# Performance work log

Measured on AMD Instinct MI355X. Metric: run time of the kernel, lower is better.

Reference implementation:

```python
import jax, jax.numpy as jnp
import numpy as np

SCALE = 64.0
DROP_P = 0.1


def setup_inputs() -> dict:
    key = jax.random.key(0)
    kq, kk, kv = jax.random.split(key, 3)
    B, Lq, Lk, D = 16, 2048, 2048, 64
    q_mat = jax.random.normal(kq, (B, Lq, D), dtype=jnp.float32)
    k_mat = jax.random.normal(kk, (B, Lk, D), dtype=jnp.float32)
    v_mat = jax.random.normal(kv, (B, Lk, D), dtype=jnp.float32)
    return {"q_mat": q_mat, "k_mat": k_mat, "v_mat": v_mat}


def reference(q_mat, k_mat, v_mat):
    # scores: [B, Lq, Lk]; note scale is a MULTIPLIER, as in the torch module
    scores = jnp.einsum('bqd,bkd->bqk', q_mat, k_mat) * SCALE
    # softmax over dim=-2, i.e. over the QUERY axis (non-standard)
    weights = jax.nn.softmax(scores, axis=-2)
    # dropout with p=0.1, training=True (fixed key for reproducibility)
    keep = jax.random.bernoulli(jax.random.key(42), 1.0 - DROP_P, weights.shape)
    weights = jnp.where(keep, weights / (1.0 - DROP_P), 0.0)
    # output: [B, Lq, D]
    return jnp.einsum('bqk,bkd->bqd', weights, v_mat)
```

## Files before the change

kernel.cpp:

```cpp
#include <hip/hip_runtime.h>
#include <stdint.h>


#define LQ 2048
#define DD 64

typedef short bf16x8 __attribute__((ext_vector_type(8)));
typedef float f32x4 __attribute__((ext_vector_type(4)));
typedef unsigned short ushort_t;

#define MFMA16(a, b, c) __builtin_amdgcn_mfma_f32_16x16x32_bf16(a, b, c, 0, 0, 0)

__device__ __forceinline__ ushort_t f2bf(float x) {
  uint32_t u = __float_as_uint(x);
  return (ushort_t)((u + 0x7FFFu + ((u >> 16) & 1u)) >> 16);
}
__device__ __forceinline__ float bf2f(ushort_t h) {
  return __uint_as_float(((uint32_t)h) << 16);
}

__device__ __forceinline__ void split8v(float4 a, float4 b, bf16x8* H, bf16x8* L) {
  float xs[8] = {a.x, a.y, a.z, a.w, b.x, b.y, b.z, b.w};
  bf16x8 h, l;
#pragma unroll
  for (int e = 0; e < 8; ++e) {
    ushort_t hh = f2bf(xs[e]);
    h[e] = (short)hh;
    l[e] = (short)f2bf(xs[e] - bf2f(hh));
  }
  *H = h; *L = l;
}

__device__ __forceinline__ f32x4 score6(bf16x8 Ah0, bf16x8 Ah1, bf16x8 Al0, bf16x8 Al1,
                                        bf16x8 Bh0, bf16x8 Bh1, bf16x8 Bl0, bf16x8 Bl1) {
  f32x4 acc = {0.f, 0.f, 0.f, 0.f};
  acc = MFMA16(Ah0, Bh0, acc);
  acc = MFMA16(Ah1, Bh1, acc);
  acc = MFMA16(Al0, Bh0, acc);
  acc = MFMA16(Al1, Bh1, acc);
  acc = MFMA16(Ah0, Bl0, acc);
  acc = MFMA16(Ah1, Bl1, acc);
  return acc;
}

__device__ __forceinline__ void stage_q(const float* __restrict__ gsrc,
                                        short (*Qh)[72], short (*Ql)[72], int tid) {
  const float4* src = (const float4*)gsrc;
#pragma unroll
  for (int i = 0; i < 4; ++i) {
    int idx = tid + (i << 8);
    int r = idx >> 4, c4 = idx & 15;
    float4 v = src[idx];
    short4 h, l;
    ushort_t t;
    t = f2bf(v.x); h.x = (short)t; l.x = (short)f2bf(v.x - bf2f(t));
    t = f2bf(v.y); h.y = (short)t; l.y = (short)f2bf(v.y - bf2f(t));
    t = f2bf(v.z); h.z = (short)t; l.z = (short)f2bf(v.z - bf2f(t));
    t = f2bf(v.w); h.w = (short)t; l.w = (short)f2bf(v.w - bf2f(t));
    *(short4*)&Qh[r][c4 * 4] = h;
    *(short4*)&Ql[r][c4 * 4] = l;
  }
}

__device__ __forceinline__ void tf_round(uint32_t& x0, uint32_t& x1, const int r) {
  x0 += x1;
  x1 = (x1 << r) | (x1 >> (32 - r));
  x1 ^= x0;
}

__device__ __forceinline__ bool keep_bit(uint32_t j) {
  const uint32_t ks1 = 42u, ks2 = 0x1BD11BDAu ^ 42u;
  uint32_t x0 = 0u;
  uint32_t x1 = j + ks1;
  tf_round(x0,x1,13); tf_round(x0,x1,15); tf_round(x0,x1,26); tf_round(x0,x1,6);
  x0 += ks1; x1 += ks2 + 1u;
  tf_round(x0,x1,17); tf_round(x0,x1,29); tf_round(x0,x1,16); tf_round(x0,x1,24);
  x0 += ks2; x1 += 0u + 2u;
  tf_round(x0,x1,13); tf_round(x0,x1,15); tf_round(x0,x1,26); tf_round(x0,x1,6);
  x0 += 0u; x1 += ks1 + 3u;
  tf_round(x0,x1,17); tf_round(x0,x1,29); tf_round(x0,x1,16); tf_round(x0,x1,24);
  x0 += ks1; x1 += ks2 + 4u;
  tf_round(x0,x1,13); tf_round(x0,x1,15); tf_round(x0,x1,26); tf_round(x0,x1,6);
  x0 += ks2; x1 += 0u + 5u;
  uint32_t bits = x0 ^ x1;
  float u = __uint_as_float((bits >> 9) | 0x3F800000u) - 1.0f;
  return u < 0.9f;
}

__global__ __launch_bounds__(256) void dotatt_colstats(
    const float* __restrict__ Q, const float* __restrict__ K,
    float* __restrict__ Mcol, float* __restrict__ Rcol) {
  __shared__ short Qh[64][72];
  __shared__ short Ql[64][72];
  const int bid = blockIdx.x;
  const int b = bid >> 5;
  const int kbase = (bid & 31) << 6;
  const int tid = threadIdx.x;
  const int lane = tid & 63;
  const int g = tid >> 6;
  const int kr = lane & 15;
  const int d0 = (lane >> 4) << 3;

  bf16x8 Bh0, Bl0, Bh1, Bl1;
  {
    const float* kp = K + ((size_t)b * LQ + kbase + (g << 4) + kr) * DD + d0;
    float4 a0 = *(const float4*)kp;
    float4 a1 = *(const float4*)(kp + 4);
    float4 a2 = *(const float4*)(kp + 32);
    float4 a3 = *(const float4*)(kp + 36);
    split8v(a0, a1, &Bh0, &Bl0);
    split8v(a2, a3, &Bh1, &Bl1);
  }

  const float* Qb = Q + (size_t)b * LQ * DD;
  float m = -1e30f, z = 0.f;

#pragma unroll 1
  for (int qt = 0; qt < 32; ++qt) {
    stage_q(Qb + (size_t)qt * 64 * DD, Qh, Ql, tid);
    __syncthreads();
    float s16[16];
#pragma unroll
    for (int qtile = 0; qtile < 4; ++qtile) {
      const int row = (qtile << 4) + kr;
      bf16x8 Ah0 = *(const bf16x8*)&Qh[row][d0];
      bf16x8 Ah1 = *(const bf16x8*)&Qh[row][d0 + 32];
      bf16x8 Al0 = *(const bf16x8*)&Ql[row][d0];
      bf16x8 Al1 = *(const bf16x8*)&Ql[row][d0 + 32];
      f32x4 s = score6(Ah0, Ah1, Al0, Al1, Bh0, Bh1, Bl0, Bl1);
#pragma unroll
      for (int r = 0; r < 4; ++r) s16[(qtile << 2) + r] = s[r] * 64.f;
    }
    __syncthreads();
    float mx = s16[0];
#pragma unroll
    for (int i = 1; i < 16; ++i) mx = fmaxf(mx, s16[i]);
    if (!__all(mx < m - 20.f)) {
      float mn = fmaxf(m, mx);
      float zz = 0.f;
#pragma unroll
      for (int i = 0; i < 16; ++i) zz += __expf(s16[i] - mn);
      z = z * __expf(m - mn) + zz;
      m = mn;
    }
  }
#pragma unroll
  for (int off = 16; off < 64; off <<= 1) {
    float om = __shfl_xor(m, off);
    float oz = __shfl_xor(z, off);
    float mn = fmaxf(m, om);
    z = z * __expf(m - mn) + oz * __expf(om - mn);
    m = mn;
  }
  if (lane < 16) {
    size_t o = (size_t)b * LQ + kbase + (g << 4) + lane;
    Mcol[o] = m;
    Rcol[o] = 1.0f / (0.9f * z);
  }
}

__global__ __launch_bounds__(256) void dotatt_out(
    const float* __restrict__ Q, const float* __restrict__ K,
    const float* __restrict__ V,
    const float* __restrict__ Mcol, const float* __restrict__ Rcol,
    float* __restrict__ Out) {
  __shared__ short Qh[64][72];
  __shared__ short Ql[64][72];
  __shared__ float Slds[4][64][17];

  const int bid = blockIdx.x;
  const int b = bid >> 5;
  const int qbase = (bid & 31) << 6;
  const int tid = threadIdx.x;
  const int lane = tid & 63;
  const int g = tid >> 6;
  const int kr = lane & 15;
  const int d0 = (lane >> 4) << 3;

  stage_q(Q + ((size_t)b * LQ + qbase) * DD, Qh, Ql, tid);
  __syncthreads();

  float acc[64];
#pragma unroll
  for (int d = 0; d < 64; ++d) acc[d] = 0.f;

  const float* Kb = K + (size_t)b * LQ * DD;
  const float* Vb = V + (size_t)b * LQ * DD;
  const float* Mb = Mcol + (size_t)b * LQ;
  const float* Rb = Rcol + (size_t)b * LQ;
  const uint32_t jrow = ((uint32_t)b * LQ + (uint32_t)(qbase + lane)) * (uint32_t)LQ;

#pragma unroll 1
  for (int t = 0; t < 32; ++t) {
    const int k0 = (g << 9) + (t << 4);
    bf16x8 Bh0, Bl0, Bh1, Bl1;
    {
      const float* kp = Kb + (size_t)(k0 + kr) * DD + d0;
      float4 a0 = *(const float4*)kp;
      float4 a1 = *(const float4*)(kp + 4);
      float4 a2 = *(const float4*)(kp + 32);
      float4 a3 = *(const float4*)(kp + 36);
      split8v(a0, a1, &Bh0, &Bl0);
      split8v(a2, a3, &Bh1, &Bl1);
    }
    const float Mw = Mb[k0 + kr];
    const float rr = Rb[k0 + kr];

    float sm[16];
#pragma unroll
    for (int qtile = 0; qtile < 4; ++qtile) {
      const int row = (qtile << 4) + kr;
      bf16x8 Ah0 = *(const bf16x8*)&Qh[row][d0];
      bf16x8 Ah1 = *(const bf16x8*)&Qh[row][d0 + 32];
      bf16x8 Al0 = *(const bf16x8*)&Ql[row][d0];
      bf16x8 Al1 = *(const bf16x8*)&Ql[row][d0 + 32];
      f32x4 s = score6(Ah0, Ah1, Al0, Al1, Bh0, Bh1, Bl0, Bl1);
#pragma unroll
      for (int r = 0; r < 4; ++r) sm[(qtile << 2) + r] = s[r] * 64.f - Mw;
    }
    float mx = sm[0];
#pragma unroll
    for (int i = 1; i < 16; ++i) mx = fmaxf(mx, sm[i]);
    if (__all(mx < -25.f)) continue;

#pragma unroll
    for (int qtile = 0; qtile < 4; ++qtile)
#pragma unroll
      for (int r = 0; r < 4; ++r)
        Slds[g][(qtile << 4) + ((lane >> 4) << 2) + r][kr] = sm[(qtile << 2) + r];

#pragma unroll 1
    for (int kk = 0; kk < 16; ++kk) {
      float smv = Slds[g][lane][kk];
      if (__all(smv < -25.f)) continue;
      float Rk = __shfl(rr, kk);
      float w = __expf(smv) * Rk;
      if (!keep_bit(jrow + (uint32_t)(k0 + kk))) w = 0.f;
      const float4* vrow = (const float4*)(Vb + (size_t)(k0 + kk) * DD);
#pragma unroll
      for (int c4 = 0; c4 < 16; ++c4) {
        float4 vv = vrow[c4];
        acc[4 * c4 + 0] += w * vv.x;
        acc[4 * c4 + 1] += w * vv.y;
        acc[4 * c4 + 2] += w * vv.z;
        acc[4 * c4 + 3] += w * vv.w;
      }
    }
  }

  __syncthreads();
  float (*qs)[68] = (float(*)[68])&Slds[0][0][0];
  for (int gg = 0; gg < 4; ++gg) {
    if (g == gg) {
      if (gg == 0) {
#pragma unroll
        for (int d = 0; d < 64; ++d) qs[lane][d] = acc[d];
      } else {
#pragma unroll
        for (int d = 0; d < 64; ++d) qs[lane][d] += acc[d];
      }
    }
    __syncthreads();
  }

  float* Ob = Out + ((size_t)b * LQ + qbase) * DD;
#pragma unroll
  for (int i = 0; i < 4; ++i) {
    int idx = tid + (i << 8);
    int r = idx >> 4, c4 = idx & 15;
    ((float4*)Ob)[idx] = *(const float4*)&qs[r][c4 * 4];
  }
}

extern "C" void kernel_launch(void* const* d_in, const int* in_sizes, int n_in,
                              void* d_out, int out_size, void* d_ws, size_t ws_size,
                              hipStream_t stream) {
  const float* Q = (const float*)d_in[0];
  const float* K = (const float*)d_in[1];
  const float* V = (const float*)d_in[2];
  float* Out  = (float*)d_out;
  float* Mcol = (float*)d_ws;
  float* Rcol = Mcol + (size_t)16 * LQ;

  hipLaunchKernelGGL(dotatt_colstats, dim3(16 * 32), dim3(256), 0, stream,
                     Q, K, Mcol, Rcol);
  hipLaunchKernelGGL(dotatt_out, dim3(16 * 32), dim3(256), 0, stream,
                     Q, K, V, Mcol, Rcol, Out);
}
```

Measured before the change: 206.0 us.

## Pre-split Q/K into bf16 hi/lo once and widen attention kernels to 512 threads

Adds a pre-pass kernel that converts Q and K into bf16 high/low halves in workspace, so the two attention kernels read bf16 fragments directly instead of re-splitting fp32 values on every tile. Both attention kernels move to 512-thread blocks. In colstats, two teams of waves each take half the query tiles and their max/sum statistics are merged through shared memory. In the output kernel, the key range is split across 8 waves, and shared Q fragments are stored in MFMA-ready order. The cost is an extra kernel launch plus extra global memory traffic for the split arrays, and more shared memory per block.

```diff
diff --git a/kernel.cpp b/kernel.cpp
--- a/kernel.cpp
+++ b/kernel.cpp
@@ -4,6 +4,7 @@
 
 #define LQ 2048
 #define DD 64
+#define NQ (16 * LQ * DD)
 
 typedef short bf16x8 __attribute__((ext_vector_type(8)));
 typedef float f32x4 __attribute__((ext_vector_type(4)));
@@ -17,18 +18,6 @@
 }
 __device__ __forceinline__ float bf2f(ushort_t h) {
   return __uint_as_float(((uint32_t)h) << 16);
-}
-
-__device__ __forceinline__ void split8v(float4 a, float4 b, bf16x8* H, bf16x8* L) {
-  float xs[8] = {a.x, a.y, a.z, a.w, b.x, b.y, b.z, b.w};
-  bf16x8 h, l;
-#pragma unroll
-  for (int e = 0; e < 8; ++e) {
-    ushort_t hh = f2bf(xs[e]);
-    h[e] = (short)hh;
-    l[e] = (short)f2bf(xs[e] - bf2f(hh));
-  }
-  *H = h; *L = l;
 }
 
 __device__ __forceinline__ f32x4 score6(bf16x8 Ah0, bf16x8 Ah1, bf16x8 Al0, bf16x8 Al1,
@@ -41,25 +30,6 @@
   acc = MFMA16(Ah0, Bl0, acc);
   acc = MFMA16(Ah1, Bl1, acc);
   return acc;
-}
-
-__device__ __forceinline__ void stage_q(const float* __restrict__ gsrc,
-                                        short (*Qh)[72], short (*Ql)[72], int tid) {
-  const float4* src = (const float4*)gsrc;
-#pragma unroll
-  for (int i = 0; i < 4; ++i) {
-    int idx = tid + (i << 8);
-    int r = idx >> 4, c4 = idx & 15;
-    float4 v = src[idx];
-    short4 h, l;
-    ushort_t t;
-    t = f2bf(v.x); h.x = (short)t; l.x = (short)f2bf(v.x - bf2f(t));
-    t = f2bf(v.y); h.y = (short)t; l.y = (short)f2bf(v.y - bf2f(t));
-    t = f2bf(v.z); h.z = (short)t; l.z = (short)f2bf(v.z - bf2f(t));
-    t = f2bf(v.w); h.w = (short)t; l.w = (short)f2bf(v.w - bf2f(t));
-    *(short4*)&Qh[r][c4 * 4] = h;
-    *(short4*)&Ql[r][c4 * 4] = l;
-  }
 }
 
 __device__ __forceinline__ void tf_round(uint32_t& x0, uint32_t& x1, const int r) {
@@ -87,11 +57,34 @@
   return u < 0.9f;
 }
 
-__global__ __launch_bounds__(256) void dotatt_colstats(
+__global__ __launch_bounds__(256) void split_qk(
     const float* __restrict__ Q, const float* __restrict__ K,
+    ushort_t* __restrict__ Qh, ushort_t* __restrict__ Ql,
+    ushort_t* __restrict__ Kh, ushort_t* __restrict__ Kl) {
+  const int total4 = (2 * NQ) / 4;
+  const int stride = 1024 * 256;
+  for (int i = blockIdx.x * 256 + threadIdx.x; i < total4; i += stride) {
+    const bool isK = i >= NQ / 4;
+    const int j = isK ? i - NQ / 4 : i;
+    float4 v = ((const float4*)(isK ? K : Q))[j];
+    short4 h, l;
+    ushort_t t;
+    t = f2bf(v.x); h.x = (short)t; l.x = (short)f2bf(v.x - bf2f(t));
+    t = f2bf(v.y); h.y = (short)t; l.y = (short)f2bf(v.y - bf2f(t));
+    t = f2bf(v.z); h.z = (short)t; l.z = (short)f2bf(v.z - bf2f(t));
+    t = f2bf(v.w); h.w = (short)t; l.w = (short)f2bf(v.w - bf2f(t));
+    *(short4*)&(isK ? Kh : Qh)[(size_t)j * 4] = h;
+    *(short4*)&(isK ? Kl : Ql)[(size_t)j * 4] = l;
+  }
+}
+
+__global__ __launch_bounds__(512) void dotatt_colstats(
+    const ushort_t* __restrict__ Qh, const ushort_t* __restrict__ Ql,
+    const ushort_t* __restrict__ Kh, const ushort_t* __restrict__ Kl,
     float* __restrict__ Mcol, float* __restrict__ Rcol) {
-  __shared__ short Qh[64][72];
-  __shared__ short Ql[64][72];
+  __shared__ ushort_t qf[2][4][4][64][8];
+  __shared__ float2 mz8[8][16];
+
   const int bid = blockIdx.x;
   const int b = bid >> 5;
   const int kbase = (bid & 31) << 6;
@@ -100,38 +93,45 @@
   const int g = tid >> 6;
   const int kr = lane & 15;
   const int d0 = (lane >> 4) << 3;
-
-  bf16x8 Bh0, Bl0, Bh1, Bl1;
-  {
-    const float* kp = K + ((size_t)b * LQ + kbase + (g << 4) + kr) * DD + d0;
-    float4 a0 = *(const float4*)kp;
-    float4 a1 = *(const float4*)(kp + 4);
-    float4 a2 = *(const float4*)(kp + 32);
-    float4 a3 = *(const float4*)(kp + 36);
-    split8v(a0, a1, &Bh0, &Bl0);
-    split8v(a2, a3, &Bh1, &Bl1);
-  }
-
-  const float* Qb = Q + (size_t)b * LQ * DD;
+  const int c = g & 3;
+  const int team = g >> 2;
+
+  const size_t krow = ((size_t)b * LQ + kbase + (c << 4) + kr) * DD;
+  bf16x8 Bh0 = *(const bf16x8*)&Kh[krow + d0];
+  bf16x8 Bh1 = *(const bf16x8*)&Kh[krow + d0 + 32];
+  bf16x8 Bl0 = *(const bf16x8*)&Kl[krow + d0];
+  bf16x8 Bl1 = *(const bf16x8*)&Kl[krow + d0 + 32];
+
+  const size_t qb = (size_t)b * LQ * DD;
   float m = -1e30f, z = 0.f;
 
 #pragma unroll 1
-  for (int qt = 0; qt < 32; ++qt) {
-    stage_q(Qb + (size_t)qt * 64 * DD, Qh, Ql, tid);
+  for (int su = 0; su < 16; ++su) {
+#pragma unroll
+    for (int i = 0; i < 4; ++i) {
+      int s = tid + (i << 9);
+      int tm = (s >> 10) & 1, qt = (s >> 8) & 3, f = (s >> 6) & 3, ln = s & 63;
+      int srow = ((su << 1) + tm) * 64 + (qt << 4) + (ln & 15);
+      int scol = ((ln >> 4) << 3) + ((f & 1) << 5);
+      const ushort_t* src = (f < 2) ? Qh : Ql;
+      *(bf16x8*)&qf[tm][qt][f][ln][0] =
+          *(const bf16x8*)&src[qb + (size_t)srow * DD + scol];
+    }
     __syncthreads();
+
     float s16[16];
 #pragma unroll
-    for (int qtile = 0; qtile < 4; ++qtile) {
-      const int row = (qtile << 4) + kr;
-      bf16x8 Ah0 = *(const bf16x8*)&Qh[row][d0];
-      bf16x8 Ah1 = *(const bf16x8*)&Qh[row][d0 + 32];
-      bf16x8 Al0 = *(const bf16x8*)&Ql[row][d0];
-      bf16x8 Al1 = *(const bf16x8*)&Ql[row][d0 + 32];
+    for (int qt = 0; qt < 4; ++qt) {
+      bf16x8 Ah0 = *(const bf16x8*)&qf[team][qt][0][lane][0];
+      bf16x8 Ah1 = *(const bf16x8*)&qf[team][qt][1][lane][0];
+      bf16x8 Al0 = *(const bf16x8*)&qf[team][qt][2][lane][0];
+      bf16x8 Al1 = *(const bf16x8*)&qf[team][qt][3][lane][0];
       f32x4 s = score6(Ah0, Ah1, Al0, Al1, Bh0, Bh1, Bl0, Bl1);
 #pragma unroll
-      for (int r = 0; r < 4; ++r) s16[(qtile << 2) + r] = s[r] * 64.f;
+      for (int r = 0; r < 4; ++r) s16[(qt << 2) + r] = s[r] * 64.f;
     }
     __syncthreads();
+
     float mx = s16[0];
 #pragma unroll
     for (int i = 1; i < 16; ++i) mx = fmaxf(mx, s16[i]);
@@ -152,21 +152,26 @@
     z = z * __expf(m - mn) + oz * __expf(om - mn);
     m = mn;
   }
-  if (lane < 16) {
+  if (lane < 16) mz8[g][lane] = make_float2(m, z);
+  __syncthreads();
+  if (g < 4 && lane < 16) {
+    float2 A = mz8[g][lane], Bv = mz8[g + 4][lane];
+    float M = fmaxf(A.x, Bv.x);
+    float Z = A.y * __expf(A.x - M) + Bv.y * __expf(Bv.x - M);
     size_t o = (size_t)b * LQ + kbase + (g << 4) + lane;
-    Mcol[o] = m;
-    Rcol[o] = 1.0f / (0.9f * z);
-  }
-}
-
-__global__ __launch_bounds__(256) void dotatt_out(
-    const float* __restrict__ Q, const float* __restrict__ K,
+    Mcol[o] = M;
+    Rcol[o] = 1.0f / (0.9f * Z);
+  }
+}
+
+__global__ __launch_bounds__(512, 4) void dotatt_out(
     const float* __restrict__ V,
+    const ushort_t* __restrict__ Qh, const ushort_t* __restrict__ Ql,
+    const ushort_t* __restrict__ Kh, const ushort_t* __restrict__ Kl,
     const float* __restrict__ Mcol, const float* __restrict__ Rcol,
     float* __restrict__ Out) {
-  __shared__ short Qh[64][72];
-  __shared__ short Ql[64][72];
-  __shared__ float Slds[4][64][17];
+  __shared__ ushort_t qf[4][4][64][8];
+  __shared__ float Slds[8][64][17];
 
   const int bid = blockIdx.x;
   const int b = bid >> 5;
@@ -175,48 +180,52 @@
   const int lane = tid & 63;
   const int g = tid >> 6;
   const int kr = lane & 15;
-  const int d0 = (lane >> 4) << 3;
-
-  stage_q(Q + ((size_t)b * LQ + qbase) * DD, Qh, Ql, tid);
+  const int hi = lane >> 4;
+  const int d0 = hi << 3;
+
+  const size_t qb = (size_t)b * LQ * DD;
+#pragma unroll
+  for (int i = 0; i < 2; ++i) {
+    int s = tid + (i << 9);
+    int qt = (s >> 8) & 3, f = (s >> 6) & 3, ln = s & 63;
+    int srow = qbase + (qt << 4) + (ln & 15);
+    int scol = ((ln >> 4) << 3) + ((f & 1) << 5);
+    const ushort_t* src = (f < 2) ? Qh : Ql;
+    *(bf16x8*)&qf[qt][f][ln][0] =
+        *(const bf16x8*)&src[qb + (size_t)srow * DD + scol];
+  }
   __syncthreads();
 
   float acc[64];
 #pragma unroll
   for (int d = 0; d < 64; ++d) acc[d] = 0.f;
 
-  const float* Kb = K + (size_t)b * LQ * DD;
-  const float* Vb = V + (size_t)b * LQ * DD;
+  const float* Vb = V + qb;
   const float* Mb = Mcol + (size_t)b * LQ;
   const float* Rb = Rcol + (size_t)b * LQ;
   const uint32_t jrow = ((uint32_t)b * LQ + (uint32_t)(qbase + lane)) * (uint32_t)LQ;
 
 #pragma unroll 1
-  for (int t = 0; t < 32; ++t) {
-    const int k0 = (g << 9) + (t << 4);
-    bf16x8 Bh0, Bl0, Bh1, Bl1;
-    {
-      const float* kp = Kb + (size_t)(k0 + kr) * DD + d0;
-      float4 a0 = *(const float4*)kp;
-      float4 a1 = *(const float4*)(kp + 4);
-      float4 a2 = *(const float4*)(kp + 32);
-      float4 a3 = *(const float4*)(kp + 36);
-      split8v(a0, a1, &Bh0, &Bl0);
-      split8v(a2, a3, &Bh1, &Bl1);
-    }
+  for (int t = 0; t < 16; ++t) {
+    const int k0 = (g << 8) + (t << 4);
+    const size_t krow = qb + (size_t)(k0 + kr) * DD;
+    bf16x8 Bh0 = *(const bf16x8*)&Kh[krow + d0];
+    bf16x8 Bh1 = *(const bf16x8*)&Kh[krow + d0 + 32];
+    bf16x8 Bl0 = *(const bf16x8*)&Kl[krow + d0];
+    bf16x8 Bl1 = *(const bf16x8*)&Kl[krow + d0 + 32];
     const float Mw = Mb[k0 + kr];
     const float rr = Rb[k0 + kr];
 
     float sm[16];
 #pragma unroll
-    for (int qtile = 0; qtile < 4; ++qtile) {
-      const int row = (qtile << 4) + kr;
-      bf16x8 Ah0 = *(const bf16x8*)&Qh[row][d0];
-      bf16x8 Ah1 = *(const bf16x8*)&Qh[row][d0 + 32];
-      bf16x8 Al0 = *(const bf16x8*)&Ql[row][d0];
-      bf16x8 Al1 = *(const bf16x8*)&Ql[row][d0 + 32];
+    for (int qt = 0; qt < 4; ++qt) {
+      bf16x8 Ah0 = *(const bf16x8*)&qf[qt][0][lane][0];
+      bf16x8 Ah1 = *(const bf16x8*)&qf[qt][1][lane][0];
+      bf16x8 Al0 = *(const bf16x8*)&qf[qt][2][lane][0];
+      bf16x8 Al1 = *(const bf16x8*)&qf[qt][3][lane][0];
       f32x4 s = score6(Ah0, Ah1, Al0, Al1, Bh0, Bh1, Bl0, Bl1);
 #pragma unroll
-      for (int r = 0; r < 4; ++r) sm[(qtile << 2) + r] = s[r] * 64.f - Mw;
+      for (int r = 0; r < 4; ++r) sm[(qt << 2) + r] = s[r] * 64.f - Mw;
     }
     float mx = sm[0];
 #pragma unroll
@@ -224,10 +233,10 @@
     if (__all(mx < -25.f)) continue;
 
 #pragma unroll
-    for (int qtile = 0; qtile < 4; ++qtile)
+    for (int qt = 0; qt < 4; ++qt)
 #pragma unroll
       for (int r = 0; r < 4; ++r)
-        Slds[g][(qtile << 4) + ((lane >> 4) << 2) + r][kr] = sm[(qtile << 2) + r];
+        Slds[g][(qt << 4) + (hi << 2) + r][kr] = sm[(qt << 2) + r];
 
 #pragma unroll 1
     for (int kk = 0; kk < 16; ++kk) {
@@ -250,7 +259,7 @@
 
   __syncthreads();
   float (*qs)[68] = (float(*)[68])&Slds[0][0][0];
-  for (int gg = 0; gg < 4; ++gg) {
+  for (int gg = 0; gg < 8; ++gg) {
     if (g == gg) {
       if (gg == 0) {
 #pragma unroll
@@ -265,8 +274,8 @@
 
   float* Ob = Out + ((size_t)b * LQ + qbase) * DD;
 #pragma unroll
-  for (int i = 0; i < 4; ++i) {
-    int idx = tid + (i << 8);
+  for (int i = 0; i < 2; ++i) {
+    int idx = tid + (i << 9);
     int r = idx >> 4, c4 = idx & 15;
     ((float4*)Ob)[idx] = *(const float4*)&qs[r][c4 * 4];
   }
@@ -278,12 +287,19 @@
   const float* Q = (const float*)d_in[0];
   const float* K = (const float*)d_in[1];
   const float* V = (const float*)d_in[2];
-  float* Out  = (float*)d_out;
-  float* Mcol = (float*)d_ws;
+  float* Out = (float*)d_out;
+
+  ushort_t* Qh = (ushort_t*)d_ws;
+  ushort_t* Ql = Qh + NQ;
+  ushort_t* Kh = Ql + NQ;
+  ushort_t* Kl = Kh + NQ;
+  float* Mcol = (float*)(Kl + NQ);
   float* Rcol = Mcol + (size_t)16 * LQ;
 
-  hipLaunchKernelGGL(dotatt_colstats, dim3(16 * 32), dim3(256), 0, stream,
-                     Q, K, Mcol, Rcol);
-  hipLaunchKernelGGL(dotatt_out, dim3(16 * 32), dim3(256), 0, stream,
-                     Q, K, V, Mcol, Rcol, Out);
-}
+  hipLaunchKernelGGL(split_qk, dim3(1024), dim3(256), 0, stream,
+                     Q, K, Qh, Ql, Kh, Kl);
+  hipLaunchKernelGGL(dotatt_colstats, dim3(16 * 32), dim3(512), 0, stream,
+                     Qh, Ql, Kh, Kl, Mcol, Rcol);
+  hipLaunchKernelGGL(dotatt_out, dim3(16 * 32), dim3(512), 0, stream,
+                     V, Qh, Ql, Kh, Kl, Mcol, Rcol, Out);
+}
```

Result: slower. 317.5 us (+54.1%).
